# Optimization experiments

Hardware: AMD Instinct MI355X
Metric: run time of the kernel (lower is better)

Reference implementation:

```python
import jax, jax.numpy as jnp
import numpy as np

ENT_N = 100000  # entity vocab (relation rows live inside this table, as in the source)
REL_N = 237
DIM = 128
N = 16384       # batch of triples
EPS = 1e-12     # F.normalize default eps


def _l2norm(x, axis=-1):
    n = jnp.linalg.norm(x, axis=axis, keepdims=True)
    return x / jnp.maximum(n, EPS)


def setup_inputs() -> dict:
    key = jax.random.key(0)
    k1, k2, k3, k4 = jax.random.split(key, 4)
    ent_emb = jax.random.normal(k1, (ENT_N, DIM), dtype=jnp.float32)
    h_ids = jax.random.randint(k2, (N,), 0, ENT_N)
    r_typ = jax.random.randint(k3, (N,), 0, REL_N)
    t_ids = jax.random.randint(k4, (N,), 0, ENT_N)
    return {"ent_emb": ent_emb, "h_ids": h_ids, "r_typ": r_typ, "t_ids": t_ids}


def reference(ent_emb, h_ids, r_typ, t_ids):
    d = ent_emb.shape[1]
    h = _l2norm(ent_emb[h_ids])           # [n, d]
    t = _l2norm(ent_emb[t_ids])           # [n, d]
    # The torch loop looks up ent_emb[r_typ*d + k] for k in range(d); gather
    # the whole relation block at once instead of d tiny lookups + cat.
    r_idx = r_typ[:, None] * d + jnp.arange(d)  # [n, d]
    R = ent_emb[r_idx]                     # [n, d, d]; row k = relation vec k
    prod = jnp.einsum('nd,nkd->nk', h, R)  # [n, d]
    prod = _l2norm(prod)
    return jnp.linalg.norm(prod - t, axis=1)  # [n]
```

## Files before the change

### kernel.cpp

```cpp
#include <hip/hip_runtime.h>

#define RELS 237
#define DIM 128
#define CH 32
#define MAXCHUNK 742
#define PREPB 64
#define MAGIC 0x5EEDF00D
#define EPS 1e-12f

typedef __attribute__((ext_vector_type(8))) short bf16x8;
typedef __attribute__((ext_vector_type(4))) float f32x4;


__device__ __forceinline__ unsigned short f2bf(float f) {
    unsigned int u = __float_as_uint(f);
    u = (u + 0x7fffu + ((u >> 16) & 1u)) >> 16;
    return (unsigned short)u;
}

__global__ __launch_bounds__(256) void k_fused(
    const float* __restrict__ ent,
    const int*   __restrict__ r_typ,
    const int*   __restrict__ h_ids,
    const int*   __restrict__ t_ids,
    int*         __restrict__ ws,
    unsigned short* __restrict__ Rc,
    int n)
{
    const int tid = threadIdx.x;

    if (blockIdx.x < RELS) {
        const int r = blockIdx.x;
        const float* src = ent + ((long)r << 14);
        unsigned short* dst = Rc + ((long)r << 14);
        #pragma unroll
        for (int s = 0; s < 8; ++s) {
            int idx = s * 256 + tid;
            int c  = idx & 15;
            int q  = (idx >> 4) & 3;
            int ks = (idx >> 6) & 3;
            int nt = idx >> 8;
            const float* sp = src + (nt * 16 + c) * 128 + ks * 32 + q * 8;
            float4 v0 = *(const float4*)sp;
            float4 v1 = *(const float4*)(sp + 4);
            uint4 wv;
            wv.x = f2bf(v0.x) | ((unsigned)f2bf(v0.y) << 16);
            wv.y = f2bf(v0.z) | ((unsigned)f2bf(v0.w) << 16);
            wv.z = f2bf(v1.x) | ((unsigned)f2bf(v1.y) << 16);
            wv.w = f2bf(v1.z) | ((unsigned)f2bf(v1.w) << 16);
            *(uint4*)(dst + (long)idx * 8) = wv;
        }
        return;
    }

    const int b = blockIdx.x - RELS;
    __shared__ int hist[256];
    __shared__ int scn[256];
    __shared__ int offsL[256];
    __shared__ int pbL[256];
    __shared__ int cursL[256];
    hist[tid] = 0;
    cursL[tid] = 0;
    __syncthreads();

    for (int i = b * 256 + tid; i < n; i += PREPB * 256)
        atomicAdd(&hist[r_typ[i]], 1);
    __syncthreads();
    ws[4096 + b * 256 + tid] = hist[tid];
    __threadfence();
    __syncthreads();
    if (tid == 0) atomicExch(&ws[2048 + b], MAGIC);

    if (tid < PREPB)
        while (atomicAdd(&ws[2048 + tid], 0) != MAGIC) __builtin_amdgcn_s_sleep(2);
    __syncthreads();

    int tot = 0, pref = 0;
    for (int bb = 0; bb < PREPB; ++bb) {
        int v = atomicAdd(&ws[4096 + bb * 256 + tid], 0);
        if (bb < b) pref += v;
        tot += v;
    }
    scn[tid] = tot; __syncthreads();
    #pragma unroll
    for (int off = 1; off < 256; off <<= 1) {
        int v = (tid >= off) ? scn[tid - off] : 0;
        __syncthreads();
        scn[tid] += v; __syncthreads();
    }
    const int offs = scn[tid] - tot;
    offsL[tid] = offs;
    pbL[tid]   = pref;
    __syncthreads();

    if (b == 0) {
        const int nch = (tot + CH - 1) >> 5;
        scn[tid] = nch; __syncthreads();
        #pragma unroll
        for (int off = 1; off < 256; off <<= 1) {
            int v = (tid >= off) ? scn[tid - off] : 0;
            __syncthreads();
            scn[tid] += v; __syncthreads();
        }
        const int choff = scn[tid] - nch;
        if (tid == 255) ws[1000] = scn[255];
        for (int j = 0; j < nch; ++j) {
            int len = tot - j * CH; if (len > CH) len = CH;
            ws[1024 + choff + j] = (tid << 20) | ((offs + j * CH) << 6) | len;
        }
    }

    for (int i = b * 256 + tid; i < n; i += PREPB * 256) {
        int rr  = r_typ[i];
        int pos = offsL[rr] + pbL[rr] + atomicAdd(&cursL[rr], 1);
        ws[32768 + pos] = i;
        ws[49152 + pos] = h_ids[i];
        ws[65536 + pos] = t_ids[i];
    }
}

__global__ __launch_bounds__(256, 4) void relgemm(
    const float*          __restrict__ ent,
    const unsigned short* __restrict__ Rc,
    const int*            __restrict__ ws,
    float*                __restrict__ out)
{
    __shared__ char smem[17152];
    unsigned short* Hb = (unsigned short*)smem;
    float* Pp  = (float*)smem;
    int*  sidx = (int*)(smem + 16896);
    int*  tRow = (int*)(smem + 17024);

    const int cid = blockIdx.x;
    if (cid >= ws[1000]) return;
    const int e    = ws[1024 + cid];
    const int r    = e >> 20;
    const int base = (e >> 6) & 16383;
    const int len  = e & 63;

    const int tid  = threadIdx.x;
    const int lane = tid & 63;
    const int w    = tid >> 6;

    if (tid < CH) {
        int tc = tid < len ? tid : len - 1;
        sidx[tid] = ws[32768 + base + tc];
        tRow[tid] = ws[65536 + base + tc];
    }

    #pragma unroll
    for (int s = 0; s < 4; ++s) {
        int g = s * 256 + tid;
        int trow = g >> 5, c4 = g & 31;
        int tc = trow < len ? trow : len - 1;
        int hid = ws[49152 + base + tc];
        float4 v = ((const float4*)ent)[((long)hid << 5) + c4];
        ushort4 bb; bb.x = f2bf(v.x); bb.y = f2bf(v.y); bb.z = f2bf(v.z); bb.w = f2bf(v.w);
        *(ushort4*)(Hb + trow * 136 + c4 * 4) = bb;
    }
    __syncthreads();

    const int q = lane >> 4, c = lane & 15;
    const unsigned short* A0p = Hb + c * 136 + q * 8;
    const unsigned short* A1p = Hb + (c + 16) * 136 + q * 8;
    const unsigned short* Bp  = Rc + ((long)r << 14) + w * 4096 + q * 128 + c * 8;

    f32x4 a00 = {0.f,0.f,0.f,0.f}, a01 = a00, a10 = a00, a11 = a00;
    #pragma unroll
    for (int ks = 0; ks < 4; ++ks) {
        bf16x8 B0 = *(const bf16x8*)(Bp + ks * 512);
        bf16x8 B1 = *(const bf16x8*)(Bp + 2048 + ks * 512);
        bf16x8 A0 = *(const bf16x8*)(A0p + ks * 32);
        bf16x8 A1 = *(const bf16x8*)(A1p + ks * 32);
        a00 = __builtin_amdgcn_mfma_f32_16x16x32_bf16(A0, B0, a00, 0, 0, 0);
        a01 = __builtin_amdgcn_mfma_f32_16x16x32_bf16(A0, B1, a01, 0, 0, 0);
        a10 = __builtin_amdgcn_mfma_f32_16x16x32_bf16(A1, B0, a10, 0, 0, 0);
        a11 = __builtin_amdgcn_mfma_f32_16x16x32_bf16(A1, B1, a11, 0, 0, 0);
    }
    __syncthreads();

    #pragma unroll
    for (int reg = 0; reg < 4; ++reg) {
        int m0 = q * 4 + reg;
        Pp[m0 * 132        + w * 32      + c] = a00[reg];
        Pp[m0 * 132        + w * 32 + 16 + c] = a01[reg];
        Pp[(m0 + 16) * 132 + w * 32      + c] = a10[reg];
        Pp[(m0 + 16) * 132 + w * 32 + 16 + c] = a11[reg];
    }
    __syncthreads();

    float p0v[8], p1v[8], t0v[8], t1v[8];
    #pragma unroll
    for (int tt = 0; tt < 8; ++tt) {
        int t = w * 8 + tt;
        int trow = tRow[t];
        const float* tv = ent + ((long)trow << 7);
        t0v[tt] = tv[lane];
        t1v[tt] = tv[lane + 64];
        p0v[tt] = Pp[t * 132 + lane];
        p1v[tt] = Pp[t * 132 + 64 + lane];
    }
    #pragma unroll
    for (int tt = 0; tt < 8; ++tt) {
        int t   = w * 8 + tt;
        float p0 = p0v[tt], p1 = p1v[tt];
        float tv0 = t0v[tt], tv1 = t1v[tt];
        float sp  = p0 * p0 + p1 * p1;
        float st  = tv0 * tv0 + tv1 * tv1;
        float spt = p0 * tv0 + p1 * tv1;
        #pragma unroll
        for (int m = 32; m >= 1; m >>= 1) {
            sp  += __shfl_xor(sp,  m, 64);
            st  += __shfl_xor(st,  m, 64);
            spt += __shfl_xor(spt, m, 64);
        }
        if (lane == 0 && t < len) {
            float npn = fmaxf(sqrtf(sp), EPS);
            float ntn = fmaxf(sqrtf(st), EPS);
            float v   = 2.0f - 2.0f * (spt / (npn * ntn));
            out[sidx[t]] = sqrtf(fmaxf(v, 0.0f));
        }
    }
}

extern "C" void kernel_launch(void* const* d_in, const int* in_sizes, int n_in,
                              void* d_out, int out_size, void* d_ws, size_t ws_size,
                              hipStream_t stream) {
    const float* ent   = (const float*)d_in[0];
    const int*   h_ids = (const int*)d_in[1];
    const int*   r_typ = (const int*)d_in[2];
    const int*   t_ids = (const int*)d_in[3];
    float* out = (float*)d_out;
    int*   ws  = (int*)d_ws;
    unsigned short* Rc = (unsigned short*)(ws + 81920);
    const int n = in_sizes[1];

    hipLaunchKernelGGL(k_fused, dim3(RELS + PREPB), dim3(256), 0, stream,
                       ent, r_typ, h_ids, t_ids, ws, Rc, n);
    hipLaunchKernelGGL(relgemm, dim3(MAXCHUNK),     dim3(256), 0, stream,
                       ent, Rc, ws, out);
}
```

Measured before the change: 114.5 us.

## Fuse prep and relation GEMM into one persistent kernel with grid barrier

Merges the conversion/bucketing kernel and the per-relation MFMA kernel into a single launch of MAXCHUNK blocks. The early blocks do the bf16 conversion and bucketing, then all blocks spin on a global flag set after every prep block signals completion. This removes one kernel launch and the gap between launches. It relies on all 742 blocks being co-resident, which at 4 blocks/CU on this GPU should hold, and stale MAGIC flags in the workspace across calls could break correctness.

New measurement: 266.8 us. +133.0%, slower.

```diff
diff --git a/kernel.cpp b/kernel.cpp
--- a/kernel.cpp
+++ b/kernel.cpp
@@ -18,15 +18,17 @@
     return (unsigned short)u;
 }
 
-__global__ __launch_bounds__(256) void k_fused(
+__global__ __launch_bounds__(256, 4) void k_all(
     const float* __restrict__ ent,
     const int*   __restrict__ r_typ,
     const int*   __restrict__ h_ids,
     const int*   __restrict__ t_ids,
     int*         __restrict__ ws,
     unsigned short* __restrict__ Rc,
+    float*       __restrict__ out,
     int n)
 {
+    __shared__ char smem[17152];
     const int tid = threadIdx.x;
 
     if (blockIdx.x < RELS) {
@@ -50,86 +52,95 @@
             wv.w = f2bf(v1.z) | ((unsigned)f2bf(v1.w) << 16);
             *(uint4*)(dst + (long)idx * 8) = wv;
         }
-        return;
-    }
-
-    const int b = blockIdx.x - RELS;
-    __shared__ int hist[256];
-    __shared__ int scn[256];
-    __shared__ int offsL[256];
-    __shared__ int pbL[256];
-    __shared__ int cursL[256];
-    hist[tid] = 0;
-    cursL[tid] = 0;
-    __syncthreads();
-
-    for (int i = b * 256 + tid; i < n; i += PREPB * 256)
-        atomicAdd(&hist[r_typ[i]], 1);
-    __syncthreads();
-    ws[4096 + b * 256 + tid] = hist[tid];
-    __threadfence();
-    __syncthreads();
-    if (tid == 0) atomicExch(&ws[2048 + b], MAGIC);
-
-    if (tid < PREPB)
-        while (atomicAdd(&ws[2048 + tid], 0) != MAGIC) __builtin_amdgcn_s_sleep(2);
-    __syncthreads();
-
-    int tot = 0, pref = 0;
-    for (int bb = 0; bb < PREPB; ++bb) {
-        int v = atomicAdd(&ws[4096 + bb * 256 + tid], 0);
-        if (bb < b) pref += v;
-        tot += v;
-    }
-    scn[tid] = tot; __syncthreads();
-    #pragma unroll
-    for (int off = 1; off < 256; off <<= 1) {
-        int v = (tid >= off) ? scn[tid - off] : 0;
-        __syncthreads();
-        scn[tid] += v; __syncthreads();
-    }
-    const int offs = scn[tid] - tot;
-    offsL[tid] = offs;
-    pbL[tid]   = pref;
-    __syncthreads();
-
-    if (b == 0) {
-        const int nch = (tot + CH - 1) >> 5;
-        scn[tid] = nch; __syncthreads();
+        __threadfence();
+        __syncthreads();
+        if (tid == 0) atomicExch(&ws[2304 + blockIdx.x], MAGIC);
+    } else if (blockIdx.x < RELS + PREPB) {
+        const int b = blockIdx.x - RELS;
+        int* hist  = (int*)smem;
+        int* scn   = (int*)(smem + 1024);
+        int* offsL = (int*)(smem + 2048);
+        int* pbL   = (int*)(smem + 3072);
+        int* cursL = (int*)(smem + 4096);
+        hist[tid] = 0;
+        cursL[tid] = 0;
+        __syncthreads();
+
+        for (int i = b * 256 + tid; i < n; i += PREPB * 256)
+            atomicAdd(&hist[r_typ[i]], 1);
+        __syncthreads();
+        ws[4096 + b * 256 + tid] = hist[tid];
+        __threadfence();
+        __syncthreads();
+        if (tid == 0) atomicExch(&ws[2048 + b], MAGIC);
+
+        if (tid < PREPB)
+            while (atomicAdd(&ws[2048 + tid], 0) != MAGIC) __builtin_amdgcn_s_sleep(2);
+        __syncthreads();
+
+        int tot = 0, pref = 0;
+        for (int bb = 0; bb < PREPB; ++bb) {
+            int v = atomicAdd(&ws[4096 + bb * 256 + tid], 0);
+            if (bb < b) pref += v;
+            tot += v;
+        }
+        scn[tid] = tot; __syncthreads();
         #pragma unroll
         for (int off = 1; off < 256; off <<= 1) {
             int v = (tid >= off) ? scn[tid - off] : 0;
             __syncthreads();
             scn[tid] += v; __syncthreads();
         }
-        const int choff = scn[tid] - nch;
-        if (tid == 255) ws[1000] = scn[255];
-        for (int j = 0; j < nch; ++j) {
-            int len = tot - j * CH; if (len > CH) len = CH;
-            ws[1024 + choff + j] = (tid << 20) | ((offs + j * CH) << 6) | len;
-        }
-    }
-
-    for (int i = b * 256 + tid; i < n; i += PREPB * 256) {
-        int rr  = r_typ[i];
-        int pos = offsL[rr] + pbL[rr] + atomicAdd(&cursL[rr], 1);
-        ws[32768 + pos] = i;
-        ws[49152 + pos] = h_ids[i];
-        ws[65536 + pos] = t_ids[i];
-    }
-}
-
-__global__ __launch_bounds__(256, 4) void relgemm(
-    const float*          __restrict__ ent,
-    const unsigned short* __restrict__ Rc,
-    const int*            __restrict__ ws,
-    float*                __restrict__ out)
-{
-    __shared__ char smem[17152];
-    unsigned short* Hb = (unsigned short*)smem;
-    float* Pp  = (float*)smem;
-    int*  sidx = (int*)(smem + 16896);
-    int*  tRow = (int*)(smem + 17024);
+        const int offs = scn[tid] - tot;
+        offsL[tid] = offs;
+        pbL[tid]   = pref;
+        __syncthreads();
+
+        if (b == 0) {
+            const int nch = (tot + CH - 1) >> 5;
+            scn[tid] = nch; __syncthreads();
+            #pragma unroll
+            for (int off = 1; off < 256; off <<= 1) {
+                int v = (tid >= off) ? scn[tid - off] : 0;
+                __syncthreads();
+                scn[tid] += v; __syncthreads();
+            }
+            const int choff = scn[tid] - nch;
+            if (tid == 255) ws[1000] = scn[255];
+            for (int j = 0; j < nch; ++j) {
+                int len = tot - j * CH; if (len > CH) len = CH;
+                ws[1024 + choff + j] = (tid << 20) | ((offs + j * CH) << 6) | len;
+            }
+        }
+
+        for (int i = b * 256 + tid; i < n; i += PREPB * 256) {
+            int rr  = r_typ[i];
+            int pos = offsL[rr] + pbL[rr] + atomicAdd(&cursL[rr], 1);
+            ws[32768 + pos] = i;
+            ws[49152 + pos] = h_ids[i];
+            ws[65536 + pos] = t_ids[i];
+        }
+        __threadfence();
+        __syncthreads();
+        if (tid == 0) atomicExch(&ws[2304 + blockIdx.x], MAGIC);
+
+        if (b == 0) {
+            for (int f = tid; f < RELS + PREPB; f += 256)
+                while (__hip_atomic_load(&ws[2304 + f], __ATOMIC_RELAXED,
+                                         __HIP_MEMORY_SCOPE_AGENT) != MAGIC)
+                    __builtin_amdgcn_s_sleep(4);
+            __syncthreads();
+            if (tid == 0) atomicExch(&ws[2800], MAGIC);
+        }
+    }
+
+    if (tid == 0) {
+        while (__hip_atomic_load(&ws[2800], __ATOMIC_ACQUIRE,
+                                 __HIP_MEMORY_SCOPE_AGENT) != MAGIC)
+            __builtin_amdgcn_s_sleep(6);
+    }
+    __syncthreads();
+    __threadfence();
 
     const int cid = blockIdx.x;
     if (cid >= ws[1000]) return;
@@ -138,7 +149,11 @@
     const int base = (e >> 6) & 16383;
     const int len  = e & 63;
 
-    const int tid  = threadIdx.x;
+    unsigned short* Hb = (unsigned short*)smem;
+    float* Pp  = (float*)smem;
+    int*  sidx = (int*)(smem + 16896);
+    int*  tRow = (int*)(smem + 17024);
+
     const int lane = tid & 63;
     const int w    = tid >> 6;
 
@@ -235,8 +250,6 @@
     unsigned short* Rc = (unsigned short*)(ws + 81920);
     const int n = in_sizes[1];
 
-    hipLaunchKernelGGL(k_fused, dim3(RELS + PREPB), dim3(256), 0, stream,
-                       ent, r_typ, h_ids, t_ids, ws, Rc, n);
-    hipLaunchKernelGGL(relgemm, dim3(MAXCHUNK),     dim3(256), 0, stream,
-                       ent, Rc, ws, out);
+    hipLaunchKernelGGL(k_all, dim3(MAXCHUNK), dim3(256), 0, stream,
+                       ent, r_typ, h_ids, t_ids, ws, Rc, out, n);
 }
```
